# Performance work log

Measured on AMD Instinct MI355X. Metric: run time of the kernel, lower is better.

The kernel has to match this reference:

```python
import jax, jax.numpy as jnp
import numpy as np

BLOCK_SIZE = 256
N_EMBD = 384
HEAD_SIZE = 384
B = 256
T = 256


def setup_inputs() -> dict:
    key = jax.random.key(0)
    kx, kk, kq, kv = jax.random.split(key, 4)
    scale = 1.0 / np.sqrt(N_EMBD)
    x = jax.random.normal(kx, (B, T, N_EMBD), dtype=jnp.float32)
    Wk = jax.random.normal(kk, (HEAD_SIZE, N_EMBD), dtype=jnp.float32) * scale
    Wq = jax.random.normal(kq, (HEAD_SIZE, N_EMBD), dtype=jnp.float32) * scale
    Wv = jax.random.normal(kv, (HEAD_SIZE, N_EMBD), dtype=jnp.float32) * scale
    return {"x": x, "Wk": Wk, "Wq": Wq, "Wv": Wv}


def reference(x, Wk, Wq, Wv):
    # Single-head causal self-attention; equals forward_with_cache at prefill
    # (fresh cache, cache_index=0, T tokens) and forward_no_cache.
    # Linear layers are bias-free: y = x @ W.T
    k = jnp.einsum('btc,hc->bth', x, Wk)  # [B,T,H]
    q = jnp.einsum('btc,hc->bth', x, Wq)
    v = jnp.einsum('btc,hc->bth', x, Wv)
    inv_sqrt_hs = jnp.asarray(HEAD_SIZE, x.dtype) ** -0.5
    wei = jnp.einsum('bth,bsh->bts', q, k) * inv_sqrt_hs  # [B,T,T]
    causal = jnp.tril(jnp.ones((T, T), dtype=bool))
    wei = jnp.where(causal, wei, jnp.asarray(-jnp.inf, wei.dtype))
    wei = jax.nn.softmax(wei, axis=-1)
    # dropout is identity in eval mode
    out = jnp.einsum('bts,bsh->bth', wei, v)  # [B,T,H]
    return out
```

## Files before the change

### kernel.cpp

```cpp
#include <hip/hip_runtime.h>

#define B_ 256
#define T_ 256
#define C_ 384
#define H_ 384

typedef float f4 __attribute__((ext_vector_type(4)));
typedef float f32x4 __attribute__((ext_vector_type(4)));
typedef short bf8 __attribute__((ext_vector_type(8)));
typedef short s8v __attribute__((ext_vector_type(8)));
typedef short s4v __attribute__((ext_vector_type(4)));

__device__ __forceinline__ short f2bf(float f) {
  unsigned u = __builtin_bit_cast(unsigned, f);
  u += 0x7FFFu + ((u >> 16) & 1u);
  return (short)(u >> 16);
}

__device__ __forceinline__ void gload_lds16(const void* g, void* l) {
  __builtin_amdgcn_global_load_lds(
      (const __attribute__((address_space(1))) unsigned int*)g,
      (__attribute__((address_space(3))) unsigned int*)l, 16, 0, 0);
}

__global__ __launch_bounds__(256) void convert_kernel(
    const float* __restrict__ x, const float* __restrict__ wk,
    const float* __restrict__ wq, const float* __restrict__ wv,
    short* __restrict__ xb, short* __restrict__ wb) {
  const int NXG = (B_ * T_ * C_) / 8;
  const int NWG = (H_ * C_) / 8;
  const int total = NXG + 3 * NWG;
  for (int g = blockIdx.x * 256 + threadIdx.x; g < total; g += gridDim.x * 256) {
    const float* src;
    short* dst;
    if (g < NXG) {
      src = x + (size_t)g * 8;
      dst = xb + (size_t)g * 8;
    } else {
      int h = g - NXG;
      int wsel = h / NWG;
      int o = h - wsel * NWG;
      const float* wp = wsel == 0 ? wk : (wsel == 1 ? wq : wv);
      src = wp + (size_t)o * 8;
      dst = wb + (size_t)wsel * (H_ * C_) + (size_t)o * 8;
    }
    f4 f0 = *(const f4*)src;
    f4 f1 = *(const f4*)(src + 4);
    s8v r;
    r[0] = f2bf(f0[0]); r[1] = f2bf(f0[1]); r[2] = f2bf(f0[2]); r[3] = f2bf(f0[3]);
    r[4] = f2bf(f1[0]); r[5] = f2bf(f1[1]); r[6] = f2bf(f1[2]); r[7] = f2bf(f1[3]);
    *(s8v*)dst = r;
  }
}

__global__ __launch_bounds__(512) void proj_gemm(
    const short* __restrict__ xb, const short* __restrict__ wb,
    short* __restrict__ kb, short* __restrict__ qbuf, short* __restrict__ vt) {
  __shared__ __align__(16) short lA[3][256 * 64];
  __shared__ __align__(16) short lB[3][128 * 64];
  const int tid = threadIdx.x;
  const int bid = blockIdx.x;
  const int swz = (bid & 7) * 288 + (bid >> 3);
  const int nb = swz % 9;
  const int mb = swz / 9;
  const int m0 = mb * 256, gn0 = nb * 128;
  const int w = tid >> 6, l = tid & 63;
  const int wr = w >> 1, wc = w & 1;

  auto STAGE = [&](int buf, int t) {
    const int k0 = t * 64;
#pragma unroll
    for (int j = 0; j < 4; ++j) {
      const int flat = j * 512 + tid;
      const int row = flat >> 3;
      const int colg = ((flat & 7) ^ (row & 7)) * 8;
      gload_lds16(xb + (size_t)(m0 + row) * C_ + k0 + colg,
                  (char*)&lA[buf][0] + flat * 16);
    }
#pragma unroll
    for (int j = 0; j < 2; ++j) {
      const int flat = j * 512 + tid;
      const int row = flat >> 3;
      const int colg = ((flat & 7) ^ (row & 7)) * 8;
      gload_lds16(wb + (size_t)(gn0 + row) * C_ + k0 + colg,
                  (char*)&lB[buf][0] + flat * 16);
    }
  };

  f32x4 acc[4][4] = {};
  STAGE(0, 0);
  STAGE(1, 1);
  STAGE(2, 2);
#pragma unroll
  for (int t = 0; t < 6; ++t) {
    const int cur = t % 3;
    if (t < 4)      asm volatile("s_waitcnt vmcnt(12)" ::: "memory");
    else if (t == 4) asm volatile("s_waitcnt vmcnt(6)" ::: "memory");
    else             asm volatile("s_waitcnt vmcnt(0)" ::: "memory");
    __builtin_amdgcn_s_barrier();
    __builtin_amdgcn_sched_barrier(0);
    const short* A = &lA[cur][0];
    const short* Bt = &lB[cur][0];
#pragma unroll
    for (int q = 0; q < 4; ++q) {
      const int mtp = q >> 1, ntp = q & 1;
      bf8 av[2][2], bv[2][2];
#pragma unroll
      for (int ks = 0; ks < 2; ++ks) {
        const int kg = ks * 4 + (l >> 4);
#pragma unroll
        for (int i = 0; i < 2; ++i) {
          const int ra = wr * 64 + (mtp * 2 + i) * 16 + (l & 15);
          av[ks][i] = *(const bf8*)&A[ra * 64 + ((kg ^ (ra & 7)) << 3)];
          const int rb = wc * 64 + (ntp * 2 + i) * 16 + (l & 15);
          bv[ks][i] = *(const bf8*)&Bt[rb * 64 + ((kg ^ (rb & 7)) << 3)];
        }
      }
      __builtin_amdgcn_s_setprio(1);
#pragma unroll
      for (int ks = 0; ks < 2; ++ks)
#pragma unroll
        for (int i = 0; i < 2; ++i)
#pragma unroll
          for (int jj = 0; jj < 2; ++jj)
            acc[mtp * 2 + i][ntp * 2 + jj] =
                __builtin_amdgcn_mfma_f32_16x16x32_bf16(
                    av[ks][i], bv[ks][jj], acc[mtp * 2 + i][ntp * 2 + jj],
                    0, 0, 0);
      __builtin_amdgcn_s_setprio(0);
    }
    __builtin_amdgcn_sched_barrier(0);
    __builtin_amdgcn_s_barrier();
    if (t < 3) STAGE(cur, t + 3);
  }
  const int proj = nb / 3;
  const int gcb = (nb % 3) * 128 + wc * 64 + (l & 15);
  const int tok0 = m0 + wr * 64 + ((l >> 4) * 4);
  if (proj < 2) {
    short* dst = proj == 0 ? kb : qbuf;
#pragma unroll
    for (int mt = 0; mt < 4; ++mt)
#pragma unroll
      for (int nt = 0; nt < 4; ++nt)
#pragma unroll
        for (int r = 0; r < 4; ++r)
          dst[(size_t)(tok0 + mt * 16 + r) * H_ + gcb + nt * 16] =
              f2bf(acc[mt][nt][r]);
  } else {
    const int bb = tok0 >> 8;
    const int tl0 = tok0 & 255;
#pragma unroll
    for (int mt = 0; mt < 4; ++mt)
#pragma unroll
      for (int nt = 0; nt < 4; ++nt) {
        s4v pk;
        pk[0] = f2bf(acc[mt][nt][0]); pk[1] = f2bf(acc[mt][nt][1]);
        pk[2] = f2bf(acc[mt][nt][2]); pk[3] = f2bf(acc[mt][nt][3]);
        *(s4v*)&vt[(size_t)bb * (H_ * T_) + (size_t)(gcb + nt * 16) * T_ +
                   tl0 + mt * 16] = pk;
      }
  }
}

__global__ __launch_bounds__(256) void attn_kernel(
    const short* __restrict__ qbuf, const short* __restrict__ kb,
    const short* __restrict__ vt, float* __restrict__ out) {
  __shared__ __align__(16) char smem[40960];
  short* Kl = (short*)smem;
  short* Ql = (short*)(smem + 32768);
  short* Pl = (short*)smem;
  const int bid = blockIdx.x;
  const int swzb = (bid & 7) * 128 + (bid >> 3);
  const int b = swzb >> 2;
  const int qi = swzb & 3;
  const int t0 = qi * 64;
  const int SKV = t0 + 64;
  const int ntile = SKV >> 4;
  const int tid = threadIdx.x;
  const int w = tid >> 6, l = tid & 63;
  f32x4 sa[16] = {};
  for (int hc = 0; hc < 6; ++hc) {
    const int h0 = hc * 64;
#pragma unroll
    for (int j = 0; j < 2; ++j) {
      const int flat = j * 256 + tid;
      const int row = flat >> 3;
      const int colg = ((flat & 7) ^ (row & 7)) * 8;
      gload_lds16(qbuf + (size_t)(b * T_ + t0 + row) * H_ + h0 + colg,
                  (char*)Ql + flat * 16);
    }
    const int kiss = SKV >> 5;
    for (int j = 0; j < kiss; ++j) {
      const int flat = j * 256 + tid;
      const int row = flat >> 3;
      const int colg = ((flat & 7) ^ (row & 7)) * 8;
      gload_lds16(kb + (size_t)(b * T_ + row) * H_ + h0 + colg,
                  (char*)Kl + flat * 16);
    }
    __syncthreads();
#pragma unroll
    for (int ks = 0; ks < 2; ++ks) {
      const int kg = ks * 4 + (l >> 4);
      const int rq = w * 16 + (l & 15);
      bf8 av = *(const bf8*)&Ql[rq * 64 + ((kg ^ (rq & 7)) << 3)];
#pragma unroll
      for (int nt = 0; nt < 16; ++nt)
        if (nt < ntile) {
          const int rk = nt * 16 + (l & 15);
          bf8 bv = *(const bf8*)&Kl[rk * 64 + ((kg ^ (rk & 7)) << 3)];
          sa[nt] = __builtin_amdgcn_mfma_f32_16x16x32_bf16(av, bv, sa[nt], 0, 0, 0);
        }
    }
    __syncthreads();
  }
  const float scale = 0.05103103630798287f;
  const int rbl = w * 16 + (l >> 4) * 4;
#pragma unroll
  for (int r = 0; r < 4; ++r) {
    const int prow = rbl + r;
    const int trow = t0 + prow;
    float vv[16];
    float m = -3.0e38f;
#pragma unroll
    for (int nt = 0; nt < 16; ++nt)
      if (nt < ntile) {
        const int col = nt * 16 + (l & 15);
        float v = sa[nt][r] * scale;
        if (col > trow) v = -3.0e38f;
        vv[nt] = v;
        m = fmaxf(m, v);
      }
    m = fmaxf(m, __shfl_xor(m, 1));
    m = fmaxf(m, __shfl_xor(m, 2));
    m = fmaxf(m, __shfl_xor(m, 4));
    m = fmaxf(m, __shfl_xor(m, 8));
    float s = 0.f;
#pragma unroll
    for (int nt = 0; nt < 16; ++nt)
      if (nt < ntile) {
        vv[nt] = __expf(vv[nt] - m);
        s += vv[nt];
      }
    s += __shfl_xor(s, 1);
    s += __shfl_xor(s, 2);
    s += __shfl_xor(s, 4);
    s += __shfl_xor(s, 8);
    const float inv = 1.0f / s;
    const int sw = (prow & 7) << 3;
#pragma unroll
    for (int nt = 0; nt < 16; ++nt)
      if (nt < ntile) {
        const int col = nt * 16 + (l & 15);
        Pl[prow * 256 + (col ^ sw)] = f2bf(vv[nt] * inv);
      }
  }
  __syncthreads();
  f32x4 o[4][6] = {};
  const int nks = SKV >> 5;
  for (int ks = 0; ks < nks; ++ks) {
    const int kk = ks * 32 + (l >> 4) * 8;
    bf8 av[4];
#pragma unroll
    for (int mt = 0; mt < 4; ++mt) {
      const int rp = mt * 16 + (l & 15);
      av[mt] = *(const bf8*)&Pl[rp * 256 + (kk ^ ((rp & 7) << 3))];
    }
#pragma unroll
    for (int nt = 0; nt < 6; ++nt) {
      const int d = w * 96 + nt * 16 + (l & 15);
      bf8 bv = *(const bf8*)&vt[(size_t)b * (H_ * T_) + (size_t)d * T_ + kk];
#pragma unroll
      for (int mt = 0; mt < 4; ++mt)
        o[mt][nt] = __builtin_amdgcn_mfma_f32_16x16x32_bf16(av[mt], bv, o[mt][nt], 0, 0, 0);
    }
  }
#pragma unroll
  for (int mt = 0; mt < 4; ++mt) {
    const int tok = b * T_ + t0 + mt * 16 + (l >> 4) * 4;
#pragma unroll
    for (int nt = 0; nt < 6; ++nt) {
      const int d = w * 96 + nt * 16 + (l & 15);
#pragma unroll
      for (int r = 0; r < 4; ++r)
        out[(size_t)(tok + r) * H_ + d] = o[mt][nt][r];
    }
  }
}

extern "C" void kernel_launch(void* const* d_in, const int* in_sizes, int n_in,
                              void* d_out, int out_size, void* d_ws, size_t ws_size,
                              hipStream_t stream) {
  (void)in_sizes; (void)n_in; (void)out_size; (void)ws_size;
  const float* x = (const float*)d_in[0];
  const float* wk = (const float*)d_in[1];
  const float* wq = (const float*)d_in[2];
  const float* wv = (const float*)d_in[3];
  float* out = (float*)d_out;
  char* ws = (char*)d_ws;
  const size_t SZ = (size_t)B_ * T_ * H_ * 2;
  short* kbuf = (short*)ws;
  short* qbuf = (short*)(ws + SZ);
  short* vt   = (short*)(ws + 2 * SZ);
  short* xb = (short*)d_out;
  short* wb = (short*)((char*)d_out + SZ);
  convert_kernel<<<2048, 256, 0, stream>>>(x, wk, wq, wv, xb, wb);
  proj_gemm<<<2304, 512, 0, stream>>>(xb, wb, kbuf, qbuf, vt);
  attn_kernel<<<1024, 256, 0, stream>>>(qbuf, kbuf, vt, out);
}
```

Baseline: 323.0 us.

## Enlarge projection GEMM tile to 512x128 with double-buffered LDS staging

The projection GEMM block tile doubles from 256x128 to 512x128 and each wave now computes a 128x64 sub-tile, which improves operand reuse per LDS load and halves the grid to 1152 blocks. Triple-buffered prefetch is replaced by double buffering: the next K-slice is issued at the top of each iteration, with a vmcnt wait for the current one. The LDS footprint grows to 160KB and the accumulator registers double. This risks lower occupancy, a shallower prefetch pipeline and a coarser last wave of blocks.

```diff
diff --git a/kernel.cpp b/kernel.cpp
--- a/kernel.cpp
+++ b/kernel.cpp
@@ -53,24 +53,24 @@
   }
 }
 
-__global__ __launch_bounds__(512) void proj_gemm(
+__global__ __launch_bounds__(512, 2) void proj_gemm(
     const short* __restrict__ xb, const short* __restrict__ wb,
     short* __restrict__ kb, short* __restrict__ qbuf, short* __restrict__ vt) {
-  __shared__ __align__(16) short lA[3][256 * 64];
-  __shared__ __align__(16) short lB[3][128 * 64];
+  __shared__ __align__(16) short lA[2][512 * 64];
+  __shared__ __align__(16) short lB[2][128 * 64];
   const int tid = threadIdx.x;
   const int bid = blockIdx.x;
-  const int swz = (bid & 7) * 288 + (bid >> 3);
+  const int swz = (bid & 7) * 144 + (bid >> 3);
   const int nb = swz % 9;
   const int mb = swz / 9;
-  const int m0 = mb * 256, gn0 = nb * 128;
+  const int m0 = mb * 512, gn0 = nb * 128;
   const int w = tid >> 6, l = tid & 63;
-  const int wr = w >> 1, wc = w & 1;
+  const int wrm = w >> 1, wcn = w & 1;
 
   auto STAGE = [&](int buf, int t) {
     const int k0 = t * 64;
 #pragma unroll
-    for (int j = 0; j < 4; ++j) {
+    for (int j = 0; j < 8; ++j) {
       const int flat = j * 512 + tid;
       const int row = flat >> 3;
       const int colg = ((flat & 7) ^ (row & 7)) * 8;
@@ -87,59 +87,54 @@
     }
   };
 
-  f32x4 acc[4][4] = {};
+  f32x4 acc[8][4] = {};
   STAGE(0, 0);
-  STAGE(1, 1);
-  STAGE(2, 2);
 #pragma unroll
   for (int t = 0; t < 6; ++t) {
-    const int cur = t % 3;
-    if (t < 4)      asm volatile("s_waitcnt vmcnt(12)" ::: "memory");
-    else if (t == 4) asm volatile("s_waitcnt vmcnt(6)" ::: "memory");
-    else             asm volatile("s_waitcnt vmcnt(0)" ::: "memory");
+    const int cur = t & 1;
+    if (t < 5) {
+      STAGE(cur ^ 1, t + 1);
+      asm volatile("s_waitcnt vmcnt(10)" ::: "memory");
+    } else {
+      asm volatile("s_waitcnt vmcnt(0)" ::: "memory");
+    }
     __builtin_amdgcn_s_barrier();
     __builtin_amdgcn_sched_barrier(0);
     const short* A = &lA[cur][0];
     const short* Bt = &lB[cur][0];
 #pragma unroll
-    for (int q = 0; q < 4; ++q) {
-      const int mtp = q >> 1, ntp = q & 1;
-      bf8 av[2][2], bv[2][2];
-#pragma unroll
-      for (int ks = 0; ks < 2; ++ks) {
-        const int kg = ks * 4 + (l >> 4);
-#pragma unroll
-        for (int i = 0; i < 2; ++i) {
-          const int ra = wr * 64 + (mtp * 2 + i) * 16 + (l & 15);
-          av[ks][i] = *(const bf8*)&A[ra * 64 + ((kg ^ (ra & 7)) << 3)];
-          const int rb = wc * 64 + (ntp * 2 + i) * 16 + (l & 15);
-          bv[ks][i] = *(const bf8*)&Bt[rb * 64 + ((kg ^ (rb & 7)) << 3)];
-        }
+    for (int ks = 0; ks < 2; ++ks) {
+      const int kg = ks * 4 + (l >> 4);
+      bf8 av[8], bv[4];
+#pragma unroll
+      for (int mt = 0; mt < 8; ++mt) {
+        const int ra = wrm * 128 + mt * 16 + (l & 15);
+        av[mt] = *(const bf8*)&A[ra * 64 + ((kg ^ (ra & 7)) << 3)];
+      }
+#pragma unroll
+      for (int nt = 0; nt < 4; ++nt) {
+        const int rb = wcn * 64 + nt * 16 + (l & 15);
+        bv[nt] = *(const bf8*)&Bt[rb * 64 + ((kg ^ (rb & 7)) << 3)];
       }
       __builtin_amdgcn_s_setprio(1);
 #pragma unroll
-      for (int ks = 0; ks < 2; ++ks)
-#pragma unroll
-        for (int i = 0; i < 2; ++i)
-#pragma unroll
-          for (int jj = 0; jj < 2; ++jj)
-            acc[mtp * 2 + i][ntp * 2 + jj] =
-                __builtin_amdgcn_mfma_f32_16x16x32_bf16(
-                    av[ks][i], bv[ks][jj], acc[mtp * 2 + i][ntp * 2 + jj],
-                    0, 0, 0);
+      for (int mt = 0; mt < 8; ++mt)
+#pragma unroll
+        for (int nt = 0; nt < 4; ++nt)
+          acc[mt][nt] = __builtin_amdgcn_mfma_f32_16x16x32_bf16(
+              av[mt], bv[nt], acc[mt][nt], 0, 0, 0);
       __builtin_amdgcn_s_setprio(0);
     }
     __builtin_amdgcn_sched_barrier(0);
     __builtin_amdgcn_s_barrier();
-    if (t < 3) STAGE(cur, t + 3);
   }
   const int proj = nb / 3;
-  const int gcb = (nb % 3) * 128 + wc * 64 + (l & 15);
-  const int tok0 = m0 + wr * 64 + ((l >> 4) * 4);
+  const int gcb = (nb % 3) * 128 + wcn * 64 + (l & 15);
+  const int tok0 = m0 + wrm * 128 + ((l >> 4) * 4);
   if (proj < 2) {
     short* dst = proj == 0 ? kb : qbuf;
 #pragma unroll
-    for (int mt = 0; mt < 4; ++mt)
+    for (int mt = 0; mt < 8; ++mt)
 #pragma unroll
       for (int nt = 0; nt < 4; ++nt)
 #pragma unroll
@@ -150,7 +145,7 @@
     const int bb = tok0 >> 8;
     const int tl0 = tok0 & 255;
 #pragma unroll
-    for (int mt = 0; mt < 4; ++mt)
+    for (int mt = 0; mt < 8; ++mt)
 #pragma unroll
       for (int nt = 0; nt < 4; ++nt) {
         s4v pk;
@@ -304,6 +299,6 @@
   short* xb = (short*)d_out;
   short* wb = (short*)((char*)d_out + SZ);
   convert_kernel<<<2048, 256, 0, stream>>>(x, wk, wq, wv, xb, wb);
-  proj_gemm<<<2304, 512, 0, stream>>>(xb, wb, kbuf, qbuf, vt);
+  proj_gemm<<<1152, 512, 0, stream>>>(xb, wb, kbuf, qbuf, vt);
   attn_kernel<<<1024, 256, 0, stream>>>(qbuf, kbuf, vt, out);
 }
```

After: 323.6 us. About the same (+0.2%).
